# Kernel optimization log

Hardware: AMD Instinct MI355X
Metric: run time of the kernel (lower is better)

The kernel has to match this reference:

```python
import jax, jax.numpy as jnp
import numpy as np

D_MODEL = 256
N_LAYERS = 6
PATCH = 160
N_CLASSES = 8
MAX_SEQ = 6000


def _layernorm(x, scale, bias, eps=1e-5):
    mu = jnp.mean(x, axis=-1, keepdims=True)
    var = jnp.var(x, axis=-1, keepdims=True)
    return (x - mu) * jax.lax.rsqrt(var + eps) * scale + bias


def _gru_layer(x, w_ih, w_hh, b_ih, b_hh):
    # x: [B,S,D]; w_ih,w_hh: [3D,D]; b_*: [3D]. PyTorch gate order: r,z,n.
    B, S, D = x.shape
    xp = jnp.einsum('bsd,gd->bsg', x, w_ih) + b_ih  # [B,S,3D], precompute input proj
    xp = jnp.swapaxes(xp, 0, 1)  # [S,B,3D]

    def step(h, xpt):
        gh = jnp.einsum('bd,gd->bg', h, w_hh) + b_hh
        xr, xz, xn = jnp.split(xpt, 3, axis=-1)
        hr, hz, hn = jnp.split(gh, 3, axis=-1)
        r = jax.nn.sigmoid(xr + hr)
        z = jax.nn.sigmoid(xz + hz)
        n = jnp.tanh(xn + r * hn)
        h_new = (1.0 - z) * n + z * h
        return h_new, h_new

    h0 = jnp.zeros((B, D), dtype=x.dtype)
    _, ys = jax.lax.scan(step, h0, xp)  # [S,B,D]
    return jnp.swapaxes(ys, 0, 1)


def setup_inputs() -> dict:
    key = jax.random.key(0)
    ks = jax.random.split(key, 16)
    D, L = D_MODEL, N_LAYERS
    s = lambda *sh: 0.02
    inp = {
        'waveform': jax.random.normal(ks[0], (32, 160000), dtype=jnp.float32) * 0.5,
        'conv_w': jax.random.normal(ks[1], (PATCH, D), dtype=jnp.float32) * (1.0 / np.sqrt(PATCH)),
        'pos_emb': jax.random.normal(ks[2], (MAX_SEQ, D), dtype=jnp.float32) * 0.02,
        'ln_scale': jnp.ones((L, D), dtype=jnp.float32),
        'ln_bias': jnp.zeros((L, D), dtype=jnp.float32),
        'w_ih': jax.random.normal(ks[3], (L, 3 * D, D), dtype=jnp.float32) * (1.0 / np.sqrt(D)),
        'w_hh': jax.random.normal(ks[4], (L, 3 * D, D), dtype=jnp.float32) * (1.0 / np.sqrt(D)),
        'b_ih': jnp.zeros((L, 3 * D), dtype=jnp.float32),
        'b_hh': jnp.zeros((L, 3 * D), dtype=jnp.float32),
        'fnorm_scale': jnp.ones((D,), dtype=jnp.float32),
        'fnorm_bias': jnp.zeros((D,), dtype=jnp.float32),
        'head_w1': jax.random.normal(ks[5], (D, D // 2), dtype=jnp.float32) * (1.0 / np.sqrt(D)),
        'head_b1': jnp.zeros((D // 2,), dtype=jnp.float32),
        'head_w2': jax.random.normal(ks[6], (D // 2, N_CLASSES), dtype=jnp.float32) * (1.0 / np.sqrt(D // 2)),
        'head_b2': jnp.zeros((N_CLASSES,), dtype=jnp.float32),
    }
    return inp


def reference(waveform, conv_w, pos_emb, ln_scale, ln_bias, w_ih, w_hh, b_ih, b_hh,
              fnorm_scale, fnorm_bias, head_w1, head_b1, head_w2, head_b2):
    B, T = waveform.shape
    S = T // PATCH
    # Conv1d(k=stride=PATCH, no bias) == patchify + matmul, then exact GELU
    x = waveform[:, : S * PATCH].reshape(B, S, PATCH)
    x = jax.nn.gelu(jnp.einsum('bsp,pd->bsd', x, conv_w), approximate=False)
    x = x + pos_emb[:S]
    for l in range(N_LAYERS):
        h = _layernorm(x, ln_scale[l], ln_bias[l])
        h = _gru_layer(h, w_ih[l], w_hh[l], b_ih[l], b_hh[l])
        x = x + h
    x = _layernorm(x, fnorm_scale, fnorm_bias)
    emb = jnp.mean(x, axis=1)  # [B,D]
    h = jax.nn.gelu(emb @ head_w1 + head_b1, approximate=False)  # dropout is eval no-op
    return h @ head_w2 + head_b2
```

## Files before the change

### kernel.cpp

```cpp
#include <hip/hip_runtime.h>
#include <math.h>

#define D 256
#define SEQ 1000
#define NB 32
#define PATCH 160
#define NL 6
#define M_TOTAL (NB * SEQ)
#define G3 (3 * D)

typedef _Float16 half8 __attribute__((ext_vector_type(8)));
typedef float f32x4 __attribute__((ext_vector_type(4)));

__device__ __forceinline__ float gelu_exact(float v) {
    return 0.5f * v * (1.0f + erff(v * 0.70710678118654752440f));
}

__device__ __forceinline__ void bar_lds() {
    asm volatile("s_waitcnt lgkmcnt(0)" ::: "memory");
    __builtin_amdgcn_s_barrier();
    asm volatile("" ::: "memory");
}

__device__ __forceinline__ float fast_sigmoid(float g) {
    float e = __builtin_amdgcn_exp2f(-1.44269504f * g);
    return __builtin_amdgcn_rcpf(1.f + e);
}
__device__ __forceinline__ float fast_tanh(float a) {
    a = fminf(fmaxf(a, -12.f), 12.f);
    float t = __builtin_amdgcn_exp2f(2.88539008f * a);
    return (t - 1.f) * __builtin_amdgcn_rcpf(t + 1.f);
}

__global__ __launch_bounds__(256) void conv_gelu_pos(
    const float* __restrict__ wav, const float* __restrict__ cw,
    const float* __restrict__ pos, float* __restrict__ x)
{
    __shared__ float As[64][33];
    __shared__ float Bs[32][65];
    const int m0 = blockIdx.x * 64;
    const int n0 = blockIdx.y * 64;
    const int tid = threadIdx.x;
    const int tx = tid & 15;
    const int ty = tid >> 4;
    float acc[4][4] = {};

    for (int kc = 0; kc < PATCH; kc += 32) {
        for (int p = 0; p < 8; ++p) {
            int mr = p * 8 + (tid >> 5);
            int kk = tid & 31;
            int m = m0 + mr;
            int b = m / SEQ, s = m % SEQ;
            As[mr][kk] = wav[(size_t)b * 160000 + (size_t)s * PATCH + kc + kk];
        }
        for (int p = 0; p < 8; ++p) {
            int kr = p * 4 + (tid >> 6);
            int nn = tid & 63;
            Bs[kr][nn] = cw[(size_t)(kc + kr) * D + n0 + nn];
        }
        __syncthreads();
        #pragma unroll
        for (int kk = 0; kk < 32; ++kk) {
            float a[4], bb[4];
            #pragma unroll
            for (int i = 0; i < 4; ++i) a[i] = As[ty * 4 + i][kk];
            #pragma unroll
            for (int j = 0; j < 4; ++j) bb[j] = Bs[kk][tx * 4 + j];
            #pragma unroll
            for (int i = 0; i < 4; ++i)
                #pragma unroll
                for (int j = 0; j < 4; ++j)
                    acc[i][j] = fmaf(a[i], bb[j], acc[i][j]);
        }
        __syncthreads();
    }
    #pragma unroll
    for (int i = 0; i < 4; ++i) {
        int m = m0 + ty * 4 + i;
        int s = m % SEQ;
        int n = n0 + tx * 4;
        float4 v;
        v.x = gelu_exact(acc[i][0]) + pos[(size_t)s * D + n + 0];
        v.y = gelu_exact(acc[i][1]) + pos[(size_t)s * D + n + 1];
        v.z = gelu_exact(acc[i][2]) + pos[(size_t)s * D + n + 2];
        v.w = gelu_exact(acc[i][3]) + pos[(size_t)s * D + n + 3];
        *(float4*)&x[(size_t)m * D + n] = v;
    }
}

__global__ __launch_bounds__(64) void row_stats(
    const float* __restrict__ x, float* __restrict__ st)
{
    const int m = blockIdx.x;
    const int t = threadIdx.x;
    const float* r = x + (size_t)m * D;
    float s = 0.f, q = 0.f;
    #pragma unroll
    for (int i = 0; i < 4; ++i) {
        float v = r[t + 64 * i];
        s += v;
        q += v * v;
    }
    #pragma unroll
    for (int o = 32; o > 0; o >>= 1) {
        s += __shfl_down(s, o);
        q += __shfl_down(q, o);
    }
    if (t == 0) {
        float mu = s * (1.f / 256.f);
        float var = q * (1.f / 256.f) - mu * mu;
        st[2 * m]     = mu;
        st[2 * m + 1] = rsqrtf(var + 1e-5f);
    }
}

__global__ __launch_bounds__(256) void ln_xp_gemm(
    const float* __restrict__ x, const float* __restrict__ st,
    const float* __restrict__ lnsc, const float* __restrict__ lnbi,
    const float* __restrict__ wih, const float* __restrict__ bih,
    float* __restrict__ xp)
{
    __shared__ float As[64][33];
    __shared__ float Bs[32][65];
    __shared__ float sc[D], bi[D];
    const int m0 = blockIdx.x * 64;
    const int n0 = blockIdx.y * 64;
    const int tid = threadIdx.x;
    const int tx = tid & 15;
    const int ty = tid >> 4;
    sc[tid] = lnsc[tid];
    bi[tid] = lnbi[tid];
    float acc[4][4] = {};

    for (int kc = 0; kc < D; kc += 32) {
        for (int p = 0; p < 8; ++p) {
            int mr = p * 8 + (tid >> 5);
            int kk = tid & 31;
            int m = m0 + mr;
            float mu = st[2 * m], rs = st[2 * m + 1];
            float v = x[(size_t)m * D + kc + kk];
            As[mr][kk] = (v - mu) * rs * sc[kc + kk] + bi[kc + kk];
        }
        for (int p = 0; p < 8; ++p) {
            int nr = p * 8 + (tid >> 5);
            int kk = tid & 31;
            Bs[kk][nr] = wih[(size_t)(n0 + nr) * D + kc + kk];
        }
        __syncthreads();
        #pragma unroll
        for (int kk = 0; kk < 32; ++kk) {
            float a[4], bb[4];
            #pragma unroll
            for (int i = 0; i < 4; ++i) a[i] = As[ty * 4 + i][kk];
            #pragma unroll
            for (int j = 0; j < 4; ++j) bb[j] = Bs[kk][tx * 4 + j];
            #pragma unroll
            for (int i = 0; i < 4; ++i)
                #pragma unroll
                for (int j = 0; j < 4; ++j)
                    acc[i][j] = fmaf(a[i], bb[j], acc[i][j]);
        }
        __syncthreads();
    }
    #pragma unroll
    for (int i = 0; i < 4; ++i) {
        int m = m0 + ty * 4 + i;
        int n = n0 + tx * 4;
        float4 v;
        v.x = acc[i][0] + bih[n + 0];
        v.y = acc[i][1] + bih[n + 1];
        v.z = acc[i][2] + bih[n + 2];
        v.w = acc[i][3] + bih[n + 3];
        *(float4*)&xp[(size_t)m * G3 + n] = v;
    }
}

__global__ __launch_bounds__(256) void pack_whh(
    const float* __restrict__ whh, unsigned int* __restrict__ wfrag)
{
    const int idx = blockIdx.x * 256 + threadIdx.x;
    const int j = idx & 3;
    const int l = (idx >> 2) & 63;
    const int c = (idx >> 8) & 7;
    const int t = idx >> 11;
    const int n = t * 16 + (l & 15);
    const int k = c * 32 + (l >> 4) * 8 + 2 * j;
    unsigned short lo = __builtin_bit_cast(unsigned short, (_Float16)whh[(size_t)n * D + k]);
    unsigned short hi = __builtin_bit_cast(unsigned short, (_Float16)whh[(size_t)n * D + k + 1]);
    wfrag[idx] = (unsigned int)lo | ((unsigned int)hi << 16);
}

__global__ __launch_bounds__(512, 1) void gru_scan_mfma(
    const float* __restrict__ xp, const unsigned int* __restrict__ wfrag,
    const float* __restrict__ bhh, float* __restrict__ x)
{
    __shared__ __align__(16) unsigned int h16_lds[D / 2];
    __shared__ float gate_lds[G3];
    const int tid  = threadIdx.x;
    const int w    = tid >> 6;
    const int l    = tid & 63;
    const int d    = tid;
    const int batch = blockIdx.x;

    half8 bf[6][8];
    {
        #pragma unroll
        for (int i = 0; i < 6; ++i)
            #pragma unroll
            for (int c = 0; c < 8; ++c) {
                const uint4 v = *(const uint4*)(
                    wfrag + ((size_t)(((w * 6 + i) * 8 + c) * 64 + l)) * 4);
                bf[i][c] = __builtin_bit_cast(half8, v);
            }
    }
    float bh_r = 0.f, bh_z = 0.f, bh_n = 0.f;
    if (tid < D) {
        bh_r = bhh[d];
        bh_z = bhh[D + d];
        bh_n = bhh[2 * D + d];
    }

    const float* xpb = xp + (size_t)batch * SEQ * G3;
    float* xb = x + (size_t)batch * SEQ * D;

    float hreg = 0.f;
    if (tid < D / 2) h16_lds[tid] = 0u;
    __syncthreads();

    const int lg = l >> 4;
    for (int t = 0; t < SEQ; ++t) {
        float xr = 0.f, xz = 0.f, xn_ = 0.f, xold = 0.f;
        if (tid < D) {
            const float* xpt = xpb + (size_t)t * G3;
            xr   = xpt[d];
            xz   = xpt[D + d];
            xn_  = xpt[2 * D + d];
            xold = xb[(size_t)t * D + d];
        }

        half8 af[8];
        #pragma unroll
        for (int c = 0; c < 8; ++c)
            af[c] = __builtin_bit_cast(half8,
                *(const uint4*)(h16_lds + 16 * c + 4 * lg));

        #pragma unroll
        for (int i = 0; i < 6; ++i) {
            f32x4 cf = {0.f, 0.f, 0.f, 0.f};
            #pragma unroll
            for (int c = 0; c < 8; ++c)
                cf = __builtin_amdgcn_mfma_f32_16x16x32_f16(af[c], bf[i][c], cf, 0, 0, 0);
            if (l < 16) gate_lds[(w * 6 + i) * 16 + l] = cf[0];
        }
        bar_lds();

        if (tid < D) {
            float ar = gate_lds[d];
            float az = gate_lds[D + d];
            float an = gate_lds[2 * D + d];
            float r = fast_sigmoid(xr + ar + bh_r);
            float z = fast_sigmoid(xz + az + bh_z);
            float n = fast_tanh(xn_ + r * (an + bh_n));
            float hnew = (1.f - z) * n + z * hreg;
            hreg = hnew;
            float hn1 = __shfl_down(hnew, 1);
            if (!(d & 1)) {
                unsigned short l0 = __builtin_bit_cast(unsigned short, (_Float16)hnew);
                unsigned short l1 = __builtin_bit_cast(unsigned short, (_Float16)hn1);
                h16_lds[d >> 1] = (unsigned int)l0 | ((unsigned int)l1 << 16);
            }
            xb[(size_t)t * D + d] = xold + hnew;
        }
        bar_lds();
    }
}

__global__ __launch_bounds__(256) void pool_ln(
    const float* __restrict__ x, const float* __restrict__ st,
    const float* __restrict__ fsc, const float* __restrict__ fbi,
    float* __restrict__ emb)
{
    const int b = blockIdx.x;
    const int d = threadIdx.x;
    float acc = 0.f;
    for (int s = 0; s < SEQ; ++s) {
        int m = b * SEQ + s;
        acc += (x[(size_t)m * D + d] - st[2 * m]) * st[2 * m + 1];
    }
    emb[b * D + d] = (acc * (1.f / (float)SEQ)) * fsc[d] + fbi[d];
}

__global__ __launch_bounds__(256) void head_mlp(
    const float* __restrict__ emb, const float* __restrict__ w1,
    const float* __restrict__ b1, const float* __restrict__ w2,
    const float* __restrict__ b2, float* __restrict__ out)
{
    __shared__ float es[NB][D + 1];
    __shared__ float h1[NB][128 + 1];
    const int t = threadIdx.x;
    for (int i = t; i < NB * D; i += 256) es[i / D][i % D] = emb[i];
    __syncthreads();
    for (int i = t; i < NB * 128; i += 256) {
        int bb = i / 128, j = i % 128;
        float a = b1[j];
        for (int k = 0; k < D; ++k) a = fmaf(es[bb][k], w1[(size_t)k * 128 + j], a);
        h1[bb][j] = gelu_exact(a);
    }
    __syncthreads();
    for (int i = t; i < NB * 8; i += 256) {
        int bb = i / 8, c = i % 8;
        float a = b2[c];
        for (int k = 0; k < 128; ++k) a = fmaf(h1[bb][k], w2[(size_t)k * 8 + c], a);
        out[i] = a;
    }
}

extern "C" void kernel_launch(void* const* d_in, const int* in_sizes, int n_in,
                              void* d_out, int out_size, void* d_ws, size_t ws_size,
                              hipStream_t stream)
{
    const float* wav  = (const float*)d_in[0];
    const float* cw   = (const float*)d_in[1];
    const float* pos  = (const float*)d_in[2];
    const float* lnsc = (const float*)d_in[3];
    const float* lnbi = (const float*)d_in[4];
    const float* wih  = (const float*)d_in[5];
    const float* whh  = (const float*)d_in[6];
    const float* bih  = (const float*)d_in[7];
    const float* bhh  = (const float*)d_in[8];
    const float* fsc  = (const float*)d_in[9];
    const float* fbi  = (const float*)d_in[10];
    const float* hw1  = (const float*)d_in[11];
    const float* hb1  = (const float*)d_in[12];
    const float* hw2  = (const float*)d_in[13];
    const float* hb2  = (const float*)d_in[14];

    float* ws    = (float*)d_ws;
    float* x     = ws;
    float* xp    = x + (size_t)M_TOTAL * D;
    float* st    = xp + (size_t)M_TOTAL * G3;
    unsigned int* wfrag = (unsigned int*)(st + 2 * M_TOTAL);
    float* emb   = (float*)(wfrag + 98304);

    conv_gelu_pos<<<dim3(M_TOTAL / 64, D / 64), 256, 0, stream>>>(wav, cw, pos, x);

    for (int l = 0; l < NL; ++l) {
        row_stats<<<M_TOTAL, 64, 0, stream>>>(x, st);
        ln_xp_gemm<<<dim3(M_TOTAL / 64, G3 / 64), 256, 0, stream>>>(
            x, st, lnsc + (size_t)l * D, lnbi + (size_t)l * D,
            wih + (size_t)l * G3 * D, bih + (size_t)l * G3, xp);
        pack_whh<<<384, 256, 0, stream>>>(whh + (size_t)l * G3 * D, wfrag);
        gru_scan_mfma<<<NB, 512, 0, stream>>>(
            xp, wfrag, bhh + (size_t)l * G3, x);
    }

    row_stats<<<M_TOTAL, 64, 0, stream>>>(x, st);
    pool_ln<<<NB, D, 0, stream>>>(x, st, fsc, fbi, emb);
    head_mlp<<<1, 256, 0, stream>>>(emb, hw1, hb1, hw2, hb2, (float*)d_out);
}
```

Measured before the change: 8.278 ms.

## Split GRU recurrent matvec: MFMA for r/z gates, VALU dot2 for n gate

```diff
diff --git a/kernel.cpp b/kernel.cpp
--- a/kernel.cpp
+++ b/kernel.cpp
@@ -31,6 +31,9 @@
     float t = __builtin_amdgcn_exp2f(2.88539008f * a);
     return (t - 1.f) * __builtin_amdgcn_rcpf(t + 1.f);
 }
+
+#define DOT(acc, w, h) asm("v_dot2_f32_f16 %0, %1, %2, %0" \
+                           : "+v"(acc) : "v"(w), "v"(h))
 
 __global__ __launch_bounds__(256) void conv_gelu_pos(
     const float* __restrict__ wav, const float* __restrict__ cw,
@@ -176,42 +179,64 @@
 }
 
 __global__ __launch_bounds__(256) void pack_whh(
-    const float* __restrict__ whh, unsigned int* __restrict__ wfrag)
+    const float* __restrict__ whh, unsigned int* __restrict__ wfrag,
+    unsigned int* __restrict__ wn16)
 {
     const int idx = blockIdx.x * 256 + threadIdx.x;
-    const int j = idx & 3;
-    const int l = (idx >> 2) & 63;
-    const int c = (idx >> 8) & 7;
-    const int t = idx >> 11;
-    const int n = t * 16 + (l & 15);
-    const int k = c * 32 + (l >> 4) * 8 + 2 * j;
-    unsigned short lo = __builtin_bit_cast(unsigned short, (_Float16)whh[(size_t)n * D + k]);
-    unsigned short hi = __builtin_bit_cast(unsigned short, (_Float16)whh[(size_t)n * D + k + 1]);
-    wfrag[idx] = (unsigned int)lo | ((unsigned int)hi << 16);
+    if (idx < 65536) {
+        const int j = idx & 3;
+        const int l = (idx >> 2) & 63;
+        const int c = (idx >> 8) & 7;
+        const int t = idx >> 11;
+        const int n = t * 16 + (l & 15);
+        const int k = c * 32 + (l >> 4) * 8 + 2 * j;
+        unsigned short lo = __builtin_bit_cast(unsigned short, (_Float16)whh[(size_t)n * D + k]);
+        unsigned short hi = __builtin_bit_cast(unsigned short, (_Float16)whh[(size_t)n * D + k + 1]);
+        wfrag[idx] = (unsigned int)lo | ((unsigned int)hi << 16);
+    } else {
+        const int m = idx - 65536;
+        const int d = m & 255;
+        const int s = m >> 8;
+        const size_t row = (size_t)(2 * D + d) * D + 2 * s;
+        unsigned short lo = __builtin_bit_cast(unsigned short, (_Float16)whh[row]);
+        unsigned short hi = __builtin_bit_cast(unsigned short, (_Float16)whh[row + 1]);
+        wn16[(size_t)s * 256 + d] = (unsigned int)lo | ((unsigned int)hi << 16);
+    }
 }
 
 __global__ __launch_bounds__(512, 1) void gru_scan_mfma(
     const float* __restrict__ xp, const unsigned int* __restrict__ wfrag,
+    const unsigned int* __restrict__ wn16,
     const float* __restrict__ bhh, float* __restrict__ x)
 {
     __shared__ __align__(16) unsigned int h16_lds[D / 2];
-    __shared__ float gate_lds[G3];
+    __shared__ float gate_lds[512];
+    __shared__ float prn[D];
     const int tid  = threadIdx.x;
     const int w    = tid >> 6;
     const int l    = tid & 63;
-    const int d    = tid;
+    const int d    = tid & 255;
+    const int kh   = tid >> 8;
     const int batch = blockIdx.x;
 
-    half8 bf[6][8];
+    half8 bf[4][8];
     {
         #pragma unroll
-        for (int i = 0; i < 6; ++i)
+        for (int i = 0; i < 4; ++i)
             #pragma unroll
             for (int c = 0; c < 8; ++c) {
                 const uint4 v = *(const uint4*)(
-                    wfrag + ((size_t)(((w * 6 + i) * 8 + c) * 64 + l)) * 4);
+                    wfrag + ((size_t)(((w * 4 + i) * 8 + c) * 64 + l)) * 4);
                 bf[i][c] = __builtin_bit_cast(half8, v);
             }
+    }
+    float wnA[32], wnB[32];
+    {
+        const unsigned int* wb = wn16 + (size_t)kh * 64 * 256 + d;
+        #pragma unroll
+        for (int j = 0; j < 32; ++j) wnA[j] = __uint_as_float(wb[(size_t)j * 256]);
+        #pragma unroll
+        for (int j = 0; j < 32; ++j) wnB[j] = __uint_as_float(wb[(size_t)(32 + j) * 256]);
     }
     float bh_r = 0.f, bh_z = 0.f, bh_n = 0.f;
     if (tid < D) {
@@ -228,6 +253,7 @@
     __syncthreads();
 
     const int lg = l >> 4;
+    const unsigned int* hp_base = h16_lds + kh * 64;
     for (int t = 0; t < SEQ; ++t) {
         float xr = 0.f, xz = 0.f, xn_ = 0.f, xold = 0.f;
         if (tid < D) {
@@ -245,22 +271,35 @@
                 *(const uint4*)(h16_lds + 16 * c + 4 * lg));
 
         #pragma unroll
-        for (int i = 0; i < 6; ++i) {
+        for (int i = 0; i < 4; ++i) {
             f32x4 cf = {0.f, 0.f, 0.f, 0.f};
             #pragma unroll
             for (int c = 0; c < 8; ++c)
                 cf = __builtin_amdgcn_mfma_f32_16x16x32_f16(af[c], bf[i][c], cf, 0, 0, 0);
-            if (l < 16) gate_lds[(w * 6 + i) * 16 + l] = cf[0];
-        }
+            if (l < 16) gate_lds[(w * 4 + i) * 16 + l] = cf[0];
+        }
+
+        float an_p = 0.f;
+        #pragma unroll
+        for (int c = 0; c < 8; ++c) {
+            uint4 hp = *(const uint4*)(hp_base + 4 * c);
+            DOT(an_p, wnA[4*c+0], hp.x); DOT(an_p, wnA[4*c+1], hp.y);
+            DOT(an_p, wnA[4*c+2], hp.z); DOT(an_p, wnA[4*c+3], hp.w);
+        }
+        #pragma unroll
+        for (int c = 0; c < 8; ++c) {
+            uint4 hp = *(const uint4*)(hp_base + 32 + 4 * c);
+            DOT(an_p, wnB[4*c+0], hp.x); DOT(an_p, wnB[4*c+1], hp.y);
+            DOT(an_p, wnB[4*c+2], hp.z); DOT(an_p, wnB[4*c+3], hp.w);
+        }
+        if (kh) prn[d] = an_p;
         bar_lds();
 
         if (tid < D) {
-            float ar = gate_lds[d];
-            float az = gate_lds[D + d];
-            float an = gate_lds[2 * D + d];
-            float r = fast_sigmoid(xr + ar + bh_r);
-            float z = fast_sigmoid(xz + az + bh_z);
-            float n = fast_tanh(xn_ + r * (an + bh_n));
+            float r = fast_sigmoid(xr + gate_lds[d]       + bh_r);
+            float z = fast_sigmoid(xz + gate_lds[256 + d] + bh_z);
+            float an = an_p + prn[d] + bh_n;
+            float n = fast_tanh(xn_ + r * an);
             float hnew = (1.f - z) * n + z * hreg;
             hreg = hnew;
             float hn1 = __shfl_down(hnew, 1);
@@ -340,6 +379,7 @@
     float* xp    = x + (size_t)M_TOTAL * D;
     float* st    = xp + (size_t)M_TOTAL * G3;
     unsigned int* wfrag = (unsigned int*)(st + 2 * M_TOTAL);
+    unsigned int* wn16  = wfrag + 65536;
     float* emb   = (float*)(wfrag + 98304);
 
     conv_gelu_pos<<<dim3(M_TOTAL / 64, D / 64), 256, 0, stream>>>(wav, cw, pos, x);
@@ -349,9 +389,9 @@
         ln_xp_gemm<<<dim3(M_TOTAL / 64, G3 / 64), 256, 0, stream>>>(
             x, st, lnsc + (size_t)l * D, lnbi + (size_t)l * D,
             wih + (size_t)l * G3 * D, bih + (size_t)l * G3, xp);
-        pack_whh<<<384, 256, 0, stream>>>(whh + (size_t)l * G3 * D, wfrag);
+        pack_whh<<<384, 256, 0, stream>>>(whh + (size_t)l * G3 * D, wfrag, wn16);
         gru_scan_mfma<<<NB, 512, 0, stream>>>(
-            xp, wfrag, bhh + (size_t)l * G3, x);
+            xp, wfrag, wn16, bhh + (size_t)l * G3, x);
     }
 
     row_stats<<<M_TOTAL, 64, 0, stream>>>(x, st);
```

Result: slower. 8.969 ms (+8.3%).
